# Performance work log

Hardware: AMD Instinct MI355X
Metric: run time of the kernel (lower is better)

## Reference

```python
import jax, jax.numpy as jnp
import numpy as np

N, E, D, H = 100000, 20000, 64, 4
NNZ = 500000
NEG_SLOPE_ATT = 0.2   # PyG HypergraphConv attention leaky_relu slope
NEG_SLOPE_FFN = 0.01  # nn.LeakyReLU default
LN_EPS = 1e-5


def setup_inputs() -> dict:
    key = jax.random.key(0)
    ks = jax.random.split(key, 10)
    s = 0.05
    return {
        "x": jax.random.normal(ks[0], (N, D), jnp.float32),
        "adj_row": jax.random.randint(ks[1], (NNZ,), 0, N),
        "adj_col": jax.random.randint(ks[2], (NNZ,), 0, E),
        "adj_val": jax.random.uniform(ks[3], (NNZ,), jnp.float32) + 0.1,
        "num_edges": E,
        "lin_w": jax.random.normal(ks[4], (H * D, D), jnp.float32) * s,
        "att": jax.random.normal(ks[5], (1, H, 2 * D), jnp.float32) * s,
        "bias": jnp.zeros((D,), jnp.float32),
        "ln1_g": jnp.ones((D,), jnp.float32),
        "ln1_b": jnp.zeros((D,), jnp.float32),
        "ln2_g": jnp.ones((D,), jnp.float32),
        "ln2_b": jnp.zeros((D,), jnp.float32),
        "w1": jax.random.normal(ks[6], (D, D), jnp.float32) * s,
        "b1": jnp.zeros((D,), jnp.float32),
        "w2": jax.random.normal(ks[7], (D, D), jnp.float32) * s,
        "b2": jnp.zeros((D,), jnp.float32),
    }


def _layer_norm(x, g, b):
    mu = jnp.mean(x, axis=-1, keepdims=True)
    var = jnp.mean((x - mu) ** 2, axis=-1, keepdims=True)
    return (x - mu) * jax.lax.rsqrt(var + LN_EPS) * g + b


def _hypergraph_layer(x, adj_row, adj_col, adj_val, num_edges,
                      lin_w, att, bias, ln1_g, ln1_b, ln2_g, ln2_b,
                      w1, b1, w2, b2):
    n = x.shape[0]
    # --- get_hyperedge_representation: omega = diag(1/colsum) @ H^T @ x ---
    colsum = jax.ops.segment_sum(adj_val, adj_col, num_segments=num_edges)  # [E]
    omega = jax.ops.segment_sum(adj_val[:, None] * x[adj_row], adj_col,
                                num_segments=num_edges) / colsum[:, None]  # [E, D]
    # --- HypergraphConv (use_attention=True, concat=False) ---
    xh = (x @ lin_w.T).reshape(n, H, D)              # [N, H, D]
    eh = (omega @ lin_w.T).reshape(num_edges, H, D)  # [E, H, D]
    att_x, att_e = att[0, :, :D], att[0, :, D:]      # [H, D] each
    s_n = jnp.einsum('nhd,hd->nh', xh, att_x)        # [N, H]
    s_e = jnp.einsum('ehd,hd->eh', eh, att_e)        # [E, H]
    alpha = jax.nn.leaky_relu(s_n[adj_row] + s_e[adj_col], NEG_SLOPE_ATT)  # [NNZ, H]
    # softmax over incidences grouped by hyperedge (attention_mode='node')
    amax = jax.ops.segment_max(alpha, adj_col, num_segments=num_edges)
    ea = jnp.exp(alpha - amax[adj_col])
    alpha = ea / jax.ops.segment_sum(ea, adj_col, num_segments=num_edges)[adj_col]
    # degree normalizations D (node) and B (hyperedge)
    d_deg = jax.ops.segment_sum(adj_val[adj_col], adj_row, num_segments=n)
    d_inv = jnp.where(d_deg > 0, 1.0 / d_deg, 0.0)
    b_deg = jax.ops.segment_sum(jnp.ones_like(adj_val), adj_col, num_segments=num_edges)
    b_inv = jnp.where(b_deg > 0, 1.0 / b_deg, 0.0)
    # pass 1: nodes -> hyperedges  (norm_i = B at target edge)
    msg1 = b_inv[adj_col][:, None, None] * xh[adj_row] * alpha[:, :, None]
    edge_out = jax.ops.segment_sum(msg1, adj_col, num_segments=num_edges)  # [E,H,D]
    # pass 2: hyperedges -> nodes  (norm_i = D at target node)
    msg2 = d_inv[adj_row][:, None, None] * edge_out[adj_col] * alpha[:, :, None]
    node_out = jax.ops.segment_sum(msg2, adj_row, num_segments=n)  # [N,H,D]
    conv = jnp.mean(node_out, axis=1) + bias  # concat=False -> head mean
    # --- residual + norm + FFN (Linear, Linear, LeakyReLU) ---
    h = _layer_norm(x + conv, ln1_g, ln1_b)
    ffn = jax.nn.leaky_relu((h @ w1.T + b1) @ w2.T + b2, NEG_SLOPE_FFN)
    return _layer_norm(h + ffn, ln2_g, ln2_b)


def reference(x, adj_row, adj_col, adj_val, num_edges, lin_w, att, bias,
              ln1_g, ln1_b, ln2_g, ln2_b, w1, b1, w2, b2):
    return _hypergraph_layer(x, adj_row, adj_col, adj_val, num_edges,
                             lin_w, att, bias, ln1_g, ln1_b, ln2_g, ln2_b,
                             w1, b1, w2, b2)
```

## Files before the change

### kernel.cpp

```cpp
#include <hip/hip_runtime.h>

#define N_NODES 100000
#define N_EDGES 20000
#define DIM 64
#define HEADS 4
#define NNZ_ 500000
#define LNEPS 1e-5f

__device__ __forceinline__ float wsum64(float v){
#pragma unroll
  for (int off = 32; off; off >>= 1) v += __shfl_xor(v, off);
  return v;
}
__device__ __forceinline__ float wmax64(float v){
#pragma unroll
  for (int off = 32; off; off >>= 1) v = fmaxf(v, __shfl_xor(v, off));
  return v;
}
__device__ __forceinline__ float lrelu2(float a){ return a > 0.f ? a : 0.2f*a; }

__global__ __launch_bounds__(256) void k_hist(const int* __restrict__ row,
                                              const int* __restrict__ col,
                                              const float* __restrict__ val,
                                              int* __restrict__ ecnt, int* __restrict__ ncnt,
                                              float* __restrict__ colsum, float* __restrict__ ddeg){
  int i = blockIdx.x*256 + threadIdx.x;
  if (i >= NNZ_) return;
  int c = col[i], r = row[i];
  atomicAdd(&ecnt[c], 1);
  atomicAdd(&ncnt[r], 1);
  atomicAdd(&colsum[c], val[i]);
  atomicAdd(&ddeg[r], val[c]);
}

__global__ __launch_bounds__(1024) void k_scanA(const int* __restrict__ cnt,
                                                int* __restrict__ ptr,
                                                int* __restrict__ bsum, int n){
  __shared__ int wsums[16];
  int idx = blockIdx.x*1024 + threadIdx.x;
  int lane = threadIdx.x & 63, wid = threadIdx.x >> 6;
  int v = (idx < n) ? cnt[idx] : 0;
  int s = v;
#pragma unroll
  for (int off = 1; off < 64; off <<= 1){
    int t = __shfl_up(s, off);
    if (lane >= off) s += t;
  }
  if (lane == 63) wsums[wid] = s;
  __syncthreads();
  if (wid == 0 && lane < 16){
    int ws = wsums[lane];
    int t = ws;
#pragma unroll
    for (int off = 1; off < 16; off <<= 1){
      int u = __shfl_up(t, off);
      if (lane >= off) t += u;
    }
    wsums[lane] = t - ws;
  }
  __syncthreads();
  if (idx < n) ptr[idx] = wsums[wid] + s - v;
  if (threadIdx.x == 1023) bsum[blockIdx.x] = wsums[15] + s;
}

__global__ __launch_bounds__(256) void k_scanB(int* __restrict__ bsum, int nb,
                                               int* __restrict__ ptr, int n){
  __shared__ int sh[256];
  int t = threadIdx.x;
  int v = (t < nb) ? bsum[t] : 0;
  sh[t] = v;
  __syncthreads();
  for (int off = 1; off < 256; off <<= 1){
    int u = (t >= off) ? sh[t-off] : 0;
    __syncthreads();
    sh[t] += u;
    __syncthreads();
  }
  if (t < nb) bsum[t] = sh[t] - v;
  if (t == nb-1) ptr[n] = sh[t];
}

__global__ __launch_bounds__(1024) void k_scanC(int* __restrict__ ptr,
                                                const int* __restrict__ bsum, int n){
  int idx = blockIdx.x*1024 + threadIdx.x;
  if (idx < n) ptr[idx] += bsum[blockIdx.x];
}

__global__ __launch_bounds__(256) void k_scatter(const int* __restrict__ row,
                                                 const int* __restrict__ col,
                                                 const float* __restrict__ val,
                                                 const int* __restrict__ colptr,
                                                 const int* __restrict__ rowptr,
                                                 int* __restrict__ ecur, int* __restrict__ ncur,
                                                 int* __restrict__ rowC, float* __restrict__ valC,
                                                 int* __restrict__ rposC, int* __restrict__ colR){
  int i = blockIdx.x*256 + threadIdx.x;
  if (i >= NNZ_) return;
  int c = col[i], r = row[i];
  int p = atomicAdd(&ecur[c], 1);
  int q = atomicAdd(&ncur[r], 1);
  int cpos = colptr[c] + p;
  int rpos = rowptr[r] + q;
  rowC[cpos] = r;
  valC[cpos] = val[i];
  rposC[cpos] = rpos;
  colR[rpos] = c;
}

__global__ __launch_bounds__(256) void k_watt(const float* __restrict__ lin_w,
                                              const float* __restrict__ att,
                                              float* __restrict__ wattx,
                                              float* __restrict__ watte){
  int j = threadIdx.x;
  int h = j >> 6;
  float sx = 0.f, se = 0.f;
#pragma unroll
  for (int d = 0; d < DIM; ++d){
    float w = lin_w[(h*DIM + d)*DIM + (j & 63)];
    sx = fmaf(att[h*2*DIM + d],       w, sx);
    se = fmaf(att[h*2*DIM + DIM + d], w, se);
  }
  wattx[j] = sx;
  watte[j] = se;
}

__global__ __launch_bounds__(256) void k_wfold(const float* __restrict__ w1,
                                               const float* __restrict__ w2,
                                               const float* __restrict__ b1,
                                               const float* __restrict__ b2,
                                               float* __restrict__ Wf,
                                               float* __restrict__ bp){
  int tid = threadIdx.x;
#pragma unroll
  for (int m = 0; m < 16; ++m){
    int idx = m*256 + tid;
    int o = idx >> 6, k = idx & 63;
    float s = 0.f;
#pragma unroll
    for (int i = 0; i < 64; ++i)
      s = fmaf(w2[o*64 + i], w1[i*64 + k], s);
    Wf[idx] = s;
  }
  if (tid < 64){
    float s = b2[tid];
#pragma unroll
    for (int i = 0; i < 64; ++i)
      s = fmaf(w2[tid*64 + i], b1[i], s);
    bp[tid] = s;
  }
}

__global__ __launch_bounds__(256) void k_pre(const float* __restrict__ x,
                                             const float* __restrict__ wattx,
                                             const float* __restrict__ watte,
                                             float4* __restrict__ snpe){
  int lane = threadIdx.x & 63, wid = threadIdx.x >> 6;
  int n = blockIdx.x*4 + wid;
  if (n >= N_NODES) return;
  float xv = x[(size_t)n*DIM + lane];
  float s0 = wsum64(xv*wattx[lane]);
  float s1 = wsum64(xv*wattx[64+lane]);
  float s2 = wsum64(xv*wattx[128+lane]);
  float s3 = wsum64(xv*wattx[192+lane]);
  float p0 = wsum64(xv*watte[lane]);
  float p1 = wsum64(xv*watte[64+lane]);
  float p2 = wsum64(xv*watte[128+lane]);
  float p3 = wsum64(xv*watte[192+lane]);
  if (lane == 0){
    snpe[2*(size_t)n    ] = make_float4(s0,s1,s2,s3);
    snpe[2*(size_t)n + 1] = make_float4(p0,p1,p2,p3);
  }
}

__global__ __launch_bounds__(256) void k_soft(const int* __restrict__ colptr,
                                              const int* __restrict__ rowC,
                                              const float* __restrict__ valC,
                                              const int* __restrict__ rposC,
                                              const float4* __restrict__ snpe,
                                              const float* __restrict__ colsum,
                                              float4* __restrict__ alphaC,
                                              float4* __restrict__ alphaR){
  int lane = threadIdx.x & 63, wid = threadIdx.x >> 6;
  int e = blockIdx.x*4 + wid;
  if (e >= N_EDGES) return;
  int s = colptr[e], cnt = colptr[e+1] - s;
  if (cnt == 0) return;
  float rcs = 1.0f / colsum[e];

  if (cnt <= 64){
    bool act = lane < cnt;
    int rp = 0; float v = 0.f;
    float4 snv = make_float4(0,0,0,0), p = make_float4(0,0,0,0);
    if (act){
      int r = rowC[s+lane];
      v = valC[s+lane];
      rp = rposC[s+lane];
      snv = snpe[2*(size_t)r];
      p   = snpe[2*(size_t)r + 1];
    }
    float se0 = wsum64(v*p.x)*rcs, se1 = wsum64(v*p.y)*rcs,
          se2 = wsum64(v*p.z)*rcs, se3 = wsum64(v*p.w)*rcs;
    float t0 = act ? lrelu2(snv.x+se0) : -1e30f;
    float t1 = act ? lrelu2(snv.y+se1) : -1e30f;
    float t2 = act ? lrelu2(snv.z+se2) : -1e30f;
    float t3 = act ? lrelu2(snv.w+se3) : -1e30f;
    float m0 = wmax64(t0), m1 = wmax64(t1), m2 = wmax64(t2), m3 = wmax64(t3);
    float e0 = act ? __expf(t0-m0) : 0.f;
    float e1 = act ? __expf(t1-m1) : 0.f;
    float e2 = act ? __expf(t2-m2) : 0.f;
    float e3 = act ? __expf(t3-m3) : 0.f;
    float q0 = wsum64(e0), q1 = wsum64(e1), q2 = wsum64(e2), q3 = wsum64(e3);
    if (act){
      float4 a = make_float4(e0/q0, e1/q1, e2/q2, e3/q3);
      alphaC[s+lane] = a;
      alphaR[rp] = a;
    }
    return;
  }
  float a0=0,a1=0,a2=0,a3=0;
  for (int base = 0; base < cnt; base += 64){
    int j = s + base + lane;
    if (base + lane < cnt){
      int r = rowC[j]; float v = valC[j];
      float4 p = snpe[2*(size_t)r + 1];
      a0 = fmaf(v,p.x,a0); a1 = fmaf(v,p.y,a1); a2 = fmaf(v,p.z,a2); a3 = fmaf(v,p.w,a3);
    }
  }
  float se0 = wsum64(a0)*rcs, se1 = wsum64(a1)*rcs, se2 = wsum64(a2)*rcs, se3 = wsum64(a3)*rcs;
  float m0=-1e30f,m1=-1e30f,m2=-1e30f,m3=-1e30f;
  for (int base = 0; base < cnt; base += 64){
    int j = s + base + lane;
    if (base + lane < cnt){
      float4 snv = snpe[2*(size_t)rowC[j]];
      m0 = fmaxf(m0, lrelu2(snv.x+se0)); m1 = fmaxf(m1, lrelu2(snv.y+se1));
      m2 = fmaxf(m2, lrelu2(snv.z+se2)); m3 = fmaxf(m3, lrelu2(snv.w+se3));
    }
  }
  m0 = wmax64(m0); m1 = wmax64(m1); m2 = wmax64(m2); m3 = wmax64(m3);
  float q0=0,q1=0,q2=0,q3=0;
  for (int base = 0; base < cnt; base += 64){
    int j = s + base + lane;
    if (base + lane < cnt){
      float4 snv = snpe[2*(size_t)rowC[j]];
      float e0 = __expf(lrelu2(snv.x+se0)-m0), e1 = __expf(lrelu2(snv.y+se1)-m1);
      float e2 = __expf(lrelu2(snv.z+se2)-m2), e3 = __expf(lrelu2(snv.w+se3)-m3);
      q0+=e0; q1+=e1; q2+=e2; q3+=e3;
      alphaC[j] = make_float4(e0,e1,e2,e3);
    }
  }
  q0 = wsum64(q0); q1 = wsum64(q1); q2 = wsum64(q2); q3 = wsum64(q3);
  float r0 = 1.f/q0, r1 = 1.f/q1, r2 = 1.f/q2, r3 = 1.f/q3;
  for (int base = 0; base < cnt; base += 64){
    int j = s + base + lane;
    if (base + lane < cnt){
      float4 a = alphaC[j];
      a = make_float4(a.x*r0, a.y*r1, a.z*r2, a.w*r3);
      alphaC[j] = a;
      alphaR[rposC[j]] = a;
    }
  }
}

__global__ __launch_bounds__(256) void k_agg(const int* __restrict__ colptr,
                                             const int* __restrict__ rowC,
                                             const float4* __restrict__ alphaC,
                                             const float* __restrict__ x,
                                             float* __restrict__ agg){
  int lane = threadIdx.x & 63, wid = threadIdx.x >> 6;
  int e = blockIdx.x*4 + wid;
  if (e >= N_EDGES) return;
  int s = colptr[e], cnt = colptr[e+1] - s;
  float acc0=0,acc1=0,acc2=0,acc3=0;
  for (int base = 0; base < cnt; base += 64){
    int m = cnt - base; if (m > 64) m = 64;
    int r = 0; float4 al = make_float4(0,0,0,0);
    if (lane < m){ r = rowC[s+base+lane]; al = alphaC[s+base+lane]; }
#pragma unroll 8
    for (int j = 0; j < m; ++j){
      int rj = __shfl(r, j);
      float b0 = __shfl(al.x, j), b1 = __shfl(al.y, j),
            b2 = __shfl(al.z, j), b3 = __shfl(al.w, j);
      float xv = x[(size_t)rj*DIM + lane];
      acc0 = fmaf(b0, xv, acc0); acc1 = fmaf(b1, xv, acc1);
      acc2 = fmaf(b2, xv, acc2); acc3 = fmaf(b3, xv, acc3);
    }
  }
  float binv = cnt > 0 ? 1.0f/(float)cnt : 0.f;
  size_t b = (size_t)e*256;
  agg[b       + lane] = acc0*binv;
  agg[b +  64 + lane] = acc1*binv;
  agg[b + 128 + lane] = acc2*binv;
  agg[b + 192 + lane] = acc3*binv;
}

__global__ __launch_bounds__(256) void k_eoT(const float* __restrict__ agg,
                                             const float* __restrict__ lin_w,
                                             float* __restrict__ eoT){
  __shared__ float L[16*260];
  int lane = threadIdx.x & 63, h = threadIdx.x >> 6;
  float w[64];
  const float4* wr = (const float4*)(lin_w + ((size_t)h*64 + lane)*64);
#pragma unroll
  for (int k = 0; k < 16; ++k){
    float4 t = wr[k];
    w[4*k] = t.x; w[4*k+1] = t.y; w[4*k+2] = t.z; w[4*k+3] = t.w;
  }
  int e0 = blockIdx.x*16;
  for (int el = 0; el < 16; ++el){
    float av = agg[(size_t)(e0+el)*256 + h*64 + lane];
    float o = 0.f;
#pragma unroll
    for (int k = 0; k < 64; ++k) o = fmaf(__shfl(av, k), w[k], o);
    L[el*260 + lane*4 + h] = o;
  }
  __syncthreads();
  int tid = threadIdx.x;
#pragma unroll
  for (int p = 0; p < 4; ++p){
    int el = p*4 + (tid >> 6);
    int f4 = tid & 63;
    float4 v = *(const float4*)(&L[el*260 + f4*4]);
    *(float4*)(eoT + (size_t)(e0+el)*256 + f4*4) = v;
  }
}

__global__ __launch_bounds__(256) void k_final2(const float* __restrict__ x,
                                                const int* __restrict__ rowptr,
                                                const int* __restrict__ colR,
                                                const float4* __restrict__ alphaR,
                                                const float* __restrict__ eoT,
                                                const float* __restrict__ ddeg,
                                                const float* __restrict__ bias,
                                                const float* __restrict__ g1,
                                                const float* __restrict__ b1g,
                                                const float* __restrict__ g2,
                                                const float* __restrict__ b2g,
                                                const float* __restrict__ Wf,
                                                const float* __restrict__ bp,
                                                float* __restrict__ out){
  int lane = threadIdx.x & 63, wid = threadIdx.x >> 6;
  float w[64];
  const float4* wr = (const float4*)(Wf + (size_t)lane*64);
#pragma unroll
  for (int k = 0; k < 16; ++k){
    float4 t = wr[k];
    w[4*k] = t.x; w[4*k+1] = t.y; w[4*k+2] = t.z; w[4*k+3] = t.w;
  }
  float biasv = bias[lane], bpv = bp[lane];
  float g1v = g1[lane], b1gv = b1g[lane], g2v = g2[lane], b2gv = b2g[lane];

  int nbase = blockIdx.x*16 + wid*4;
  float hs[4];

#pragma unroll
  for (int j = 0; j < 4; ++j){
    int n = nbase + j;
    int s = rowptr[n], cnt = rowptr[n+1] - s;
    float a0=0,a1=0,a2=0,a3=0;
    for (int base = 0; base < cnt; base += 64){
      int m = cnt - base; if (m > 64) m = 64;
      int c = 0; float4 al = make_float4(0,0,0,0);
      if (lane < m){ c = colR[s+base+lane]; al = alphaR[s+base+lane]; }
#pragma unroll 4
      for (int i = 0; i < m; ++i){
        int ci = __shfl(c, i);
        float q0 = __shfl(al.x, i), q1 = __shfl(al.y, i),
              q2 = __shfl(al.z, i), q3 = __shfl(al.w, i);
        const float4 v = *(const float4*)(eoT + (size_t)ci*256 + lane*4);
        a0 = fmaf(v.x, q0, a0);
        a1 = fmaf(v.y, q1, a1);
        a2 = fmaf(v.z, q2, a2);
        a3 = fmaf(v.w, q3, a3);
      }
    }
    float dd = ddeg[n];
    float dinv = dd > 0.f ? 0.25f/dd : 0.f;
    float conv = (a0+a1+a2+a3)*dinv;
    float t = x[(size_t)n*DIM + lane] + conv + biasv;
    float mu = wsum64(t) * (1.f/64.f);
    float dv = t - mu;
    float var = wsum64(dv*dv) * (1.f/64.f);
    hs[j] = dv * rsqrtf(var + LNEPS) * g1v + b1gv;
  }

  float a0 = bpv, a1 = bpv, a2 = bpv, a3 = bpv;
#pragma unroll
  for (int k = 0; k < 64; ++k){
    a0 = fmaf(__shfl(hs[0], k), w[k], a0);
    a1 = fmaf(__shfl(hs[1], k), w[k], a1);
    a2 = fmaf(__shfl(hs[2], k), w[k], a2);
    a3 = fmaf(__shfl(hs[3], k), w[k], a3);
  }

  float fa[4] = {a0, a1, a2, a3};
#pragma unroll
  for (int j = 0; j < 4; ++j){
    int n = nbase + j;
    float ffn = fa[j] > 0.f ? fa[j] : 0.01f*fa[j];
    float t2 = hs[j] + ffn;
    float mu2 = wsum64(t2) * (1.f/64.f);
    float dv2 = t2 - mu2;
    float var2 = wsum64(dv2*dv2) * (1.f/64.f);
    out[(size_t)n*DIM + lane] = dv2 * rsqrtf(var2 + LNEPS) * g2v + b2gv;
  }
}

extern "C" void kernel_launch(void* const* d_in, const int* in_sizes, int n_in,
                              void* d_out, int out_size, void* d_ws, size_t ws_size,
                              hipStream_t stream){
  const float* x     = (const float*)d_in[0];
  const int*   row   = (const int*)d_in[1];
  const int*   col   = (const int*)d_in[2];
  const float* val   = (const float*)d_in[3];
  const float* lin_w = (const float*)d_in[5];
  const float* att   = (const float*)d_in[6];
  const float* bias  = (const float*)d_in[7];
  const float* g1    = (const float*)d_in[8];
  const float* b1g   = (const float*)d_in[9];
  const float* g2    = (const float*)d_in[10];
  const float* b2g   = (const float*)d_in[11];
  const float* w1    = (const float*)d_in[12];
  const float* b1    = (const float*)d_in[13];
  const float* w2    = (const float*)d_in[14];
  const float* b2    = (const float*)d_in[15];
  float* out = (float*)d_out;
  float* ws  = (float*)d_ws;

  constexpr size_t E = N_EDGES, Nn = N_NODES;
  constexpr size_t o_ecnt   = 0;
  constexpr size_t o_ncnt   = o_ecnt + E;
  constexpr size_t o_ecur   = o_ncnt + Nn;
  constexpr size_t o_ncur   = o_ecur + E;
  constexpr size_t o_colsum = o_ncur + Nn;
  constexpr size_t o_ddeg   = o_colsum + E;
  constexpr size_t ZEND     = o_ddeg + Nn;
  constexpr size_t o_colptr = ZEND;
  constexpr size_t o_rowptr = o_colptr + E + 4;
  constexpr size_t o_bsumE  = o_rowptr + Nn + 4;
  constexpr size_t o_bsumN  = o_bsumE + 256;
  constexpr size_t o_rowC   = o_bsumN + 256;
  constexpr size_t o_valC   = o_rowC + NNZ_;
  constexpr size_t o_rposC  = o_valC + NNZ_;
  constexpr size_t o_colR   = o_rposC + NNZ_;
  constexpr size_t o_wattx  = o_colR + NNZ_;
  constexpr size_t o_watte  = o_wattx + 256;
  constexpr size_t o_Wf     = o_watte + 256;
  constexpr size_t o_bp     = o_Wf + 4096;
  constexpr size_t o_snpe   = o_bp + 64;
  constexpr size_t o_alphaC = o_snpe + 8*Nn;
  constexpr size_t o_alphaR = o_alphaC + 4*(size_t)NNZ_;
  constexpr size_t o_agg    = o_alphaR + 4*(size_t)NNZ_;
  constexpr size_t o_eo     = o_agg + 256*E;

  int*    ecnt   = (int*)(ws + o_ecnt);
  int*    ncnt   = (int*)(ws + o_ncnt);
  int*    ecur   = (int*)(ws + o_ecur);
  int*    ncur   = (int*)(ws + o_ncur);
  float*  colsum = ws + o_colsum;
  float*  ddeg   = ws + o_ddeg;
  int*    colptr = (int*)(ws + o_colptr);
  int*    rowptr = (int*)(ws + o_rowptr);
  int*    bsumE  = (int*)(ws + o_bsumE);
  int*    bsumN  = (int*)(ws + o_bsumN);
  int*    rowC   = (int*)(ws + o_rowC);
  float*  valC   = ws + o_valC;
  int*    rposC  = (int*)(ws + o_rposC);
  int*    colR   = (int*)(ws + o_colR);
  float*  wattx  = ws + o_wattx;
  float*  watte  = ws + o_watte;
  float*  Wf     = ws + o_Wf;
  float*  bp     = ws + o_bp;
  float4* snpe   = (float4*)(ws + o_snpe);
  float4* alphaC = (float4*)(ws + o_alphaC);
  float4* alphaR = (float4*)(ws + o_alphaR);
  float*  agg    = ws + o_agg;
  float*  eoT    = ws + o_eo;

  hipMemsetAsync(ws, 0, ZEND*sizeof(float), stream);

  k_hist<<<(NNZ_+255)/256, 256, 0, stream>>>(row, col, val, ecnt, ncnt, colsum, ddeg);

  int nbE = (int)((E + 1023)/1024);
  int nbN = (int)((Nn + 1023)/1024);
  k_scanA<<<nbE, 1024, 0, stream>>>(ecnt, colptr, bsumE, (int)E);
  k_scanB<<<1, 256, 0, stream>>>(bsumE, nbE, colptr, (int)E);
  k_scanC<<<nbE, 1024, 0, stream>>>(colptr, bsumE, (int)E);
  k_scanA<<<nbN, 1024, 0, stream>>>(ncnt, rowptr, bsumN, (int)Nn);
  k_scanB<<<1, 256, 0, stream>>>(bsumN, nbN, rowptr, (int)Nn);
  k_scanC<<<nbN, 1024, 0, stream>>>(rowptr, bsumN, (int)Nn);

  k_scatter<<<(NNZ_+255)/256, 256, 0, stream>>>(row, col, val, colptr, rowptr,
                                                ecur, ncur, rowC, valC, rposC, colR);

  k_watt<<<1, 256, 0, stream>>>(lin_w, att, wattx, watte);
  k_wfold<<<1, 256, 0, stream>>>(w1, w2, b1, b2, Wf, bp);
  k_pre<<<(int)((Nn+3)/4), 256, 0, stream>>>(x, wattx, watte, snpe);
  k_soft<<<(int)((E+3)/4), 256, 0, stream>>>(colptr, rowC, valC, rposC, snpe, colsum, alphaC, alphaR);
  k_agg<<<(int)((E+3)/4), 256, 0, stream>>>(colptr, rowC, alphaC, x, agg);
  k_eoT<<<(int)(E/16), 256, 0, stream>>>(agg, lin_w, eoT);
  k_final2<<<(int)(Nn/16), 256, 0, stream>>>(x, rowptr, colR, alphaR, eoT, ddeg,
                                             bias, g1, b1g, g2, b2g, Wf, bp, out);
}
```

Measured before the change: 533.1 us.

## Store edge outputs in bf16 and batch four nodes' gathers in final kernel

The per-edge transformed features (eoT) are now packed to bf16 with round-to-nearest-even, halving the bytes written by k_eoT and gathered in k_final2. k_final2 also loads the neighbor lists of its four nodes in one coalesced read when they total at most 64 entries. It then interleaves their gathers so more independent loads are in flight. This trades precision of the intermediate for bandwidth and latency hiding, and may drift from the fp32 reference tolerance.

```diff
diff --git a/kernel.cpp b/kernel.cpp
--- a/kernel.cpp
+++ b/kernel.cpp
@@ -18,6 +18,13 @@
   return v;
 }
 __device__ __forceinline__ float lrelu2(float a){ return a > 0.f ? a : 0.2f*a; }
+
+__device__ __forceinline__ unsigned bfpack(float a, float b){
+  unsigned ua = __float_as_uint(a), ub = __float_as_uint(b);
+  ua += 0x7fffu + ((ua >> 16) & 1u);
+  ub += 0x7fffu + ((ub >> 16) & 1u);
+  return (ua >> 16) | (ub & 0xffff0000u);
+}
 
 __global__ __launch_bounds__(256) void k_hist(const int* __restrict__ row,
                                               const int* __restrict__ col,
@@ -295,7 +302,7 @@
 
 __global__ __launch_bounds__(256) void k_eoT(const float* __restrict__ agg,
                                              const float* __restrict__ lin_w,
-                                             float* __restrict__ eoT){
+                                             unsigned short* __restrict__ eoTb){
   __shared__ float L[16*260];
   int lane = threadIdx.x & 63, h = threadIdx.x >> 6;
   float w[64];
@@ -318,9 +325,12 @@
 #pragma unroll
   for (int p = 0; p < 4; ++p){
     int el = p*4 + (tid >> 6);
-    int f4 = tid & 63;
-    float4 v = *(const float4*)(&L[el*260 + f4*4]);
-    *(float4*)(eoT + (size_t)(e0+el)*256 + f4*4) = v;
+    int l = tid & 63;
+    const float* Lr = &L[el*260 + l*4];
+    uint2 v;
+    v.x = bfpack(Lr[0], Lr[1]);
+    v.y = bfpack(Lr[2], Lr[3]);
+    *(uint2*)(eoTb + (size_t)(e0+el)*256 + l*4) = v;
   }
 }
 
@@ -328,7 +338,7 @@
                                                 const int* __restrict__ rowptr,
                                                 const int* __restrict__ colR,
                                                 const float4* __restrict__ alphaR,
-                                                const float* __restrict__ eoT,
+                                                const unsigned short* __restrict__ eoTb,
                                                 const float* __restrict__ ddeg,
                                                 const float* __restrict__ bias,
                                                 const float* __restrict__ g1,
@@ -350,32 +360,79 @@
   float g1v = g1[lane], b1gv = b1g[lane], g2v = g2[lane], b2gv = b2g[lane];
 
   int nbase = blockIdx.x*16 + wid*4;
+  int p0 = rowptr[nbase], p1 = rowptr[nbase+1], p2 = rowptr[nbase+2],
+      p3 = rowptr[nbase+3], p4 = rowptr[nbase+4];
+  int total = p4 - p0;
+  int cj0 = p1-p0, cj1 = p2-p1, cj2 = p3-p2, cj3 = p4-p3;
+  int oj0 = 0, oj1 = p1-p0, oj2 = p2-p0, oj3 = p3-p0;
+
+  float acc[4][4];
+#pragma unroll
+  for (int j = 0; j < 4; ++j)
+#pragma unroll
+    for (int h = 0; h < 4; ++h) acc[j][h] = 0.f;
+
+  if (total <= 64){
+    int ce = 0; float4 alv = make_float4(0,0,0,0);
+    if (lane < total){ ce = colR[p0+lane]; alv = alphaR[p0+lane]; }
+    int maxc = max(max(cj0,cj1), max(cj2,cj3));
+    int cj[4] = {cj0,cj1,cj2,cj3};
+    int oj[4] = {oj0,oj1,oj2,oj3};
+    for (int k = 0; k < maxc; ++k){
+#pragma unroll
+      for (int j = 0; j < 4; ++j){
+        if (k < cj[j]){
+          int idx = oj[j] + k;
+          int ci = __shfl(ce, idx);
+          float q0 = __shfl(alv.x, idx), q1 = __shfl(alv.y, idx),
+                q2 = __shfl(alv.z, idx), q3 = __shfl(alv.w, idx);
+          uint2 v = *(const uint2*)(eoTb + (size_t)ci*256 + lane*4);
+          float v0 = __uint_as_float(v.x << 16);
+          float v1 = __uint_as_float(v.x & 0xffff0000u);
+          float v2 = __uint_as_float(v.y << 16);
+          float v3 = __uint_as_float(v.y & 0xffff0000u);
+          acc[j][0] = fmaf(v0, q0, acc[j][0]);
+          acc[j][1] = fmaf(v1, q1, acc[j][1]);
+          acc[j][2] = fmaf(v2, q2, acc[j][2]);
+          acc[j][3] = fmaf(v3, q3, acc[j][3]);
+        }
+      }
+    }
+  } else {
+    int sj[4] = {p0, p1, p2, p3};
+    int cj[4] = {cj0,cj1,cj2,cj3};
+#pragma unroll
+    for (int j = 0; j < 4; ++j){
+      int s = sj[j], cnt = cj[j];
+      for (int base = 0; base < cnt; base += 64){
+        int m = cnt - base; if (m > 64) m = 64;
+        int c = 0; float4 al = make_float4(0,0,0,0);
+        if (lane < m){ c = colR[s+base+lane]; al = alphaR[s+base+lane]; }
+        for (int i = 0; i < m; ++i){
+          int ci = __shfl(c, i);
+          float q0 = __shfl(al.x, i), q1 = __shfl(al.y, i),
+                q2 = __shfl(al.z, i), q3 = __shfl(al.w, i);
+          uint2 v = *(const uint2*)(eoTb + (size_t)ci*256 + lane*4);
+          float v0 = __uint_as_float(v.x << 16);
+          float v1 = __uint_as_float(v.x & 0xffff0000u);
+          float v2 = __uint_as_float(v.y << 16);
+          float v3 = __uint_as_float(v.y & 0xffff0000u);
+          acc[j][0] = fmaf(v0, q0, acc[j][0]);
+          acc[j][1] = fmaf(v1, q1, acc[j][1]);
+          acc[j][2] = fmaf(v2, q2, acc[j][2]);
+          acc[j][3] = fmaf(v3, q3, acc[j][3]);
+        }
+      }
+    }
+  }
+
   float hs[4];
-
 #pragma unroll
   for (int j = 0; j < 4; ++j){
     int n = nbase + j;
-    int s = rowptr[n], cnt = rowptr[n+1] - s;
-    float a0=0,a1=0,a2=0,a3=0;
-    for (int base = 0; base < cnt; base += 64){
-      int m = cnt - base; if (m > 64) m = 64;
-      int c = 0; float4 al = make_float4(0,0,0,0);
-      if (lane < m){ c = colR[s+base+lane]; al = alphaR[s+base+lane]; }
-#pragma unroll 4
-      for (int i = 0; i < m; ++i){
-        int ci = __shfl(c, i);
-        float q0 = __shfl(al.x, i), q1 = __shfl(al.y, i),
-              q2 = __shfl(al.z, i), q3 = __shfl(al.w, i);
-        const float4 v = *(const float4*)(eoT + (size_t)ci*256 + lane*4);
-        a0 = fmaf(v.x, q0, a0);
-        a1 = fmaf(v.y, q1, a1);
-        a2 = fmaf(v.z, q2, a2);
-        a3 = fmaf(v.w, q3, a3);
-      }
-    }
     float dd = ddeg[n];
     float dinv = dd > 0.f ? 0.25f/dd : 0.f;
-    float conv = (a0+a1+a2+a3)*dinv;
+    float conv = (acc[j][0]+acc[j][1]+acc[j][2]+acc[j][3])*dinv;
     float t = x[(size_t)n*DIM + lane] + conv + biasv;
     float mu = wsum64(t) * (1.f/64.f);
     float dv = t - mu;
@@ -474,7 +531,7 @@
   float4* alphaC = (float4*)(ws + o_alphaC);
   float4* alphaR = (float4*)(ws + o_alphaR);
   float*  agg    = ws + o_agg;
-  float*  eoT    = ws + o_eo;
+  unsigned short* eoTb = (unsigned short*)(ws + o_eo);
 
   hipMemsetAsync(ws, 0, ZEND*sizeof(float), stream);
 
@@ -497,7 +554,7 @@
   k_pre<<<(int)((Nn+3)/4), 256, 0, stream>>>(x, wattx, watte, snpe);
   k_soft<<<(int)((E+3)/4), 256, 0, stream>>>(colptr, rowC, valC, rposC, snpe, colsum, alphaC, alphaR);
   k_agg<<<(int)((E+3)/4), 256, 0, stream>>>(colptr, rowC, alphaC, x, agg);
-  k_eoT<<<(int)(E/16), 256, 0, stream>>>(agg, lin_w, eoT);
-  k_final2<<<(int)(Nn/16), 256, 0, stream>>>(x, rowptr, colR, alphaR, eoT, ddeg,
+  k_eoT<<<(int)(E/16), 256, 0, stream>>>(agg, lin_w, eoTb);
+  k_final2<<<(int)(Nn/16), 256, 0, stream>>>(x, rowptr, colR, alphaR, eoTb, ddeg,
                                              bias, g1, b1g, g2, b2g, Wf, bp, out);
 }
```

New measurement: 526.3 us. No clear change (-1.3%).
